# Performance work log

Hardware: AMD Instinct MI355X
Metric: run time of the kernel (lower is better)

The kernel has to match this reference:

```python
import jax, jax.numpy as jnp
import numpy as np

B, N, C, H, L = 4, 1024, 1152, 16, 120
D = C // H
HID = 4 * C
EPS = 1e-6


def _ln(x):
    m = jnp.mean(x, axis=-1, keepdims=True)
    v = jnp.var(x, axis=-1, keepdims=True)
    return (x - m) * jax.lax.rsqrt(v + EPS)


def _attend(q, k, v):
    # q:(B,H,Nq,D) k,v:(B,H,Nk,D)
    scale = D ** -0.5
    s = jnp.einsum('bhnd,bhmd->bhnm', q, k) * scale
    p = jax.nn.softmax(s, axis=-1)
    o = jnp.einsum('bhnm,bhmd->bhnd', p, v)
    return o.transpose(0, 2, 1, 3).reshape(q.shape[0], q.shape[2], C)


def setup_inputs() -> dict:
    key = jax.random.key(0)
    ks = jax.random.split(key, 20)
    g = lambda i, shape, s=0.02: jax.random.normal(ks[i], shape, jnp.float32) * s
    return {
        'x': jax.random.normal(ks[0], (B, N, C), jnp.float32),
        'y': jax.random.normal(ks[1], (B, L, C), jnp.float32),
        't': jax.random.normal(ks[2], (B, 6 * C), jnp.float32),
        'sst': jax.random.normal(ks[3], (6, C), jnp.float32) / C ** 0.5,
        'qkv_w': g(4, (C, 3 * C)), 'qkv_b': jnp.zeros((3 * C,), jnp.float32),
        'proj_w': g(5, (C, C)), 'proj_b': jnp.zeros((C,), jnp.float32),
        'q_w': g(6, (C, C)), 'q_b': jnp.zeros((C,), jnp.float32),
        'kv_w': g(7, (C, 2 * C)), 'kv_b': jnp.zeros((2 * C,), jnp.float32),
        'cproj_w': g(8, (C, C)), 'cproj_b': jnp.zeros((C,), jnp.float32),
        'fc1_w': g(9, (C, HID)), 'fc1_b': jnp.zeros((HID,), jnp.float32),
        'fc2_w': g(10, (HID, C)), 'fc2_b': jnp.zeros((C,), jnp.float32),
    }


def reference(x, y, t, sst, qkv_w, qkv_b, proj_w, proj_b, q_w, q_b,
              kv_w, kv_b, cproj_w, cproj_b, fc1_w, fc1_b, fc2_w, fc2_b):
    mods = sst[None] + t.reshape(B, 6, C)  # (B,6,C)
    sh_msa, sc_msa, g_msa, sh_mlp, sc_mlp, g_mlp = [mods[:, i:i + 1] for i in range(6)]

    # --- self attention with adaLN modulation ---
    h = _ln(x) * (1 + sc_msa) + sh_msa
    qkv = (h @ qkv_w + qkv_b).reshape(B, N, 3, H, D).transpose(2, 0, 3, 1, 4)
    attn_out = _attend(qkv[0], qkv[1], qkv[2]) @ proj_w + proj_b
    x = x + g_msa * attn_out

    # --- cross attention (batched cond, no mask) ---
    q = (x @ q_w + q_b).reshape(B, N, H, D).transpose(0, 2, 1, 3)
    kv = (y @ kv_w + kv_b).reshape(B, L, 2, H, D).transpose(2, 0, 3, 1, 4)
    x = x + (_attend(q, kv[0], kv[1]) @ cproj_w + cproj_b)

    # --- MLP with adaLN modulation ---
    h = _ln(x) * (1 + sc_mlp) + sh_mlp
    h = jax.nn.gelu(h @ fc1_w + fc1_b, approximate=True) @ fc2_w + fc2_b
    x = x + g_mlp * h
    return x
```

## Files before the change

### kernel.cpp

```cpp
#include <hip/hip_runtime.h>
#include <hip/hip_bf16.h>
#include <stdint.h>

typedef __hip_bfloat16 BT;
typedef __bf16 bf16x8 __attribute__((ext_vector_type(8)));
typedef float f32x4 __attribute__((ext_vector_type(4)));

constexpr int kB = 4, kN = 1024, kC = 1152, kH = 16, kL = 120, kD = 72, kDp = 96;
constexpr int kHid = 4608, kBN = 4096, kZ = 64;
constexpr float kScale = 0.11785113019775793f;

__global__ void detect_dtype(const void* xin, int* flag) {
  __shared__ int cnt;
  if (threadIdx.x == 0) cnt = 0;
  __syncthreads();
  const BT* xb = (const BT*)xin;
  int local = 0;
  for (int i = threadIdx.x; i < 4096; i += 256) {
    float v = __bfloat162float(xb[i]);
    if (!(fabsf(v) <= 1e3f)) local++;
  }
  atomicAdd(&cnt, local);
  __syncthreads();
  if (threadIdx.x == 0) *flag = (cnt > 8) ? 1 : 0;
}

struct ConvSeg {
  const void* src;
  BT* dst;
  long long n;
};
struct ConvArgs {
  ConvSeg seg[10];
  int nseg;
};
__global__ void convert_all(ConvArgs a, const int* __restrict__ flag) {
  const int f = *flag;
  long long i = (long long)blockIdx.x * 256 + threadIdx.x;
#pragma unroll
  for (int s = 0; s < 10; ++s) {
    if (s >= a.nseg) return;
    if (i < a.seg[s].n) {
      a.seg[s].dst[i] = f ? __float2bfloat16(((const float*)a.seg[s].src)[i])
                          : ((const BT*)a.seg[s].src)[i];
      return;
    }
    i -= a.seg[s].n;
  }
}

__global__ void encode_ws(float* out, long long n, float c) {
  long long i = (long long)blockIdx.x * 256 + threadIdx.x;
  if (i < n) out[i] = c;
}

__device__ __forceinline__ void gl_lds16(const BT* g, BT* l) {
  __builtin_amdgcn_global_load_lds(
      (const __attribute__((address_space(1))) uint32_t*)g,
      (__attribute__((address_space(3))) uint32_t*)l, 16, 0, 0);
}

__global__ __launch_bounds__(256, 2) void flash_self(
    const BT* __restrict__ Qp, const BT* __restrict__ Kp, const BT* __restrict__ VT,
    BT* __restrict__ O) {
  const int z = blockIdx.y;
  const int q0 = blockIdx.x * 64;
  const BT* Qb = Qp + (size_t)z * kN * kDp;
  const BT* Kb = Kp + (size_t)z * kN * kDp;
  const BT* Vb = VT + (size_t)z * kD * kN;
  BT* Ob = O + (size_t)z * kN * kD;

  __shared__ __align__(16) BT Pl[64][136];
  __shared__ float redm[2][64], reds[2][64], scl[64], lsh[64];

  const int lane = threadIdx.x & 63, w = threadIdx.x >> 6;
  const int l15 = lane & 15, g8 = (lane >> 4) * 8, rowq = (lane >> 4) * 4;
  const int wm = (w & 1) * 32, wn = (w >> 1) * 64;
  const int half = w >> 1;
  const int orow = w * 16;

  bf16x8 afQ[3][2];
#pragma unroll
  for (int ks = 0; ks < 3; ++ks)
#pragma unroll
    for (int i = 0; i < 2; ++i)
      afQ[ks][i] = *reinterpret_cast<const bf16x8*>(
          &Qb[(size_t)(q0 + wm + i * 16 + l15) * kDp + ks * 32 + g8]);

  float mst[2][4], lst[2][4];
#pragma unroll
  for (int i = 0; i < 2; ++i)
#pragma unroll
    for (int r = 0; r < 4; ++r) {
      mst[i][r] = -1e30f;
      lst[i][r] = 0.f;
    }

  f32x4 accO[5] = {};

  for (int t = 0; t < 8; ++t) {
    const int kv0 = t * 128;
    f32x4 accS[2][4] = {};
#pragma unroll
    for (int ks = 0; ks < 3; ++ks) {
      bf16x8 bfK[4];
#pragma unroll
      for (int j = 0; j < 4; ++j)
        bfK[j] = *reinterpret_cast<const bf16x8*>(
            &Kb[(size_t)(kv0 + wn + j * 16 + l15) * kDp + ks * 32 + g8]);
#pragma unroll
      for (int i = 0; i < 2; ++i)
#pragma unroll
        for (int j = 0; j < 4; ++j)
          accS[i][j] = __builtin_amdgcn_mfma_f32_16x16x32_bf16(afQ[ks][i], bfK[j], accS[i][j], 0, 0, 0);
    }
    float tmax[2][4];
#pragma unroll
    for (int i = 0; i < 2; ++i)
#pragma unroll
      for (int r = 0; r < 4; ++r) {
        float v = fmaxf(fmaxf(accS[i][0][r], accS[i][1][r]),
                        fmaxf(accS[i][2][r], accS[i][3][r]));
        v = fmaxf(v, __shfl_xor(v, 1, 16));
        v = fmaxf(v, __shfl_xor(v, 2, 16));
        v = fmaxf(v, __shfl_xor(v, 4, 16));
        v = fmaxf(v, __shfl_xor(v, 8, 16));
        tmax[i][r] = v;
      }
    if (l15 == 0) {
#pragma unroll
      for (int i = 0; i < 2; ++i)
#pragma unroll
        for (int r = 0; r < 4; ++r)
          redm[half][wm + i * 16 + rowq + r] = tmax[i][r];
    }
    __syncthreads();

    float sc[2][4], tsum[2][4];
#pragma unroll
    for (int i = 0; i < 2; ++i)
#pragma unroll
      for (int r = 0; r < 4; ++r) {
        const int row = wm + i * 16 + rowq + r;
        const float mt = fmaxf(redm[0][row], redm[1][row]);
        const float mn = fmaxf(mst[i][r], mt);
        sc[i][r] = __expf(mst[i][r] - mn);
        mst[i][r] = mn;
        float s = 0.f;
#pragma unroll
        for (int j = 0; j < 4; ++j) {
          float pv = __expf(accS[i][j][r] - mn);
          s += pv;
          Pl[row][wn + j * 16 + l15] = __float2bfloat16(pv);
        }
        s += __shfl_xor(s, 1, 16);
        s += __shfl_xor(s, 2, 16);
        s += __shfl_xor(s, 4, 16);
        s += __shfl_xor(s, 8, 16);
        tsum[i][r] = s;
      }
    if (l15 == 0) {
#pragma unroll
      for (int i = 0; i < 2; ++i)
#pragma unroll
        for (int r = 0; r < 4; ++r) {
          const int row = wm + i * 16 + rowq + r;
          reds[half][row] = tsum[i][r];
          if (half == 0) scl[row] = sc[i][r];
        }
    }
    __syncthreads();

#pragma unroll
    for (int i = 0; i < 2; ++i)
#pragma unroll
      for (int r = 0; r < 4; ++r) {
        const int row = wm + i * 16 + rowq + r;
        lst[i][r] = lst[i][r] * sc[i][r] + (reds[0][row] + reds[1][row]);
      }
    float osc[4];
#pragma unroll
    for (int r = 0; r < 4; ++r) osc[r] = scl[orow + rowq + r];
#pragma unroll
    for (int jv = 0; jv < 5; ++jv)
#pragma unroll
      for (int r = 0; r < 4; ++r) accO[jv][r] *= osc[r];
#pragma unroll
    for (int ks = 0; ks < 4; ++ks) {
      bf16x8 aP = *reinterpret_cast<const bf16x8*>(&Pl[orow + l15][ks * 32 + g8]);
      bf16x8 bV[5];
#pragma unroll
      for (int jv = 0; jv < 5; ++jv)
        bV[jv] = *reinterpret_cast<const bf16x8*>(
            &Vb[(size_t)(jv * 16 + l15) * kN + kv0 + ks * 32 + g8]);
#pragma unroll
      for (int jv = 0; jv < 5; ++jv)
        accO[jv] = __builtin_amdgcn_mfma_f32_16x16x32_bf16(aP, bV[jv], accO[jv], 0, 0, 0);
    }
  }

  if (half == 0 && l15 == 0) {
#pragma unroll
    for (int i = 0; i < 2; ++i)
#pragma unroll
      for (int r = 0; r < 4; ++r)
        lsh[wm + i * 16 + rowq + r] = lst[i][r];
  }
  __syncthreads();
  float linv[4];
#pragma unroll
  for (int r = 0; r < 4; ++r) linv[r] = 1.f / lsh[orow + rowq + r];
#pragma unroll
  for (int jv = 0; jv < 5; ++jv) {
    const int d = jv * 16 + l15;
    if (d < kD) {
#pragma unroll
      for (int r = 0; r < 4; ++r)
        Ob[(size_t)(q0 + orow + rowq + r) * kD + d] =
            __float2bfloat16(accO[jv][r] * linv[r]);
    }
  }
}

template <int EP>
__global__ __launch_bounds__(512, 2) void gemm_w8(
    const BT* __restrict__ A, const BT* __restrict__ Bm, const BT* __restrict__ bias,
    void* __restrict__ Cout, int M, int Nc, int K, int lda, int ldb, int ldc,
    long long sA, long long sB, long long sC) {
  __shared__ __align__(16) BT As[2][128 * 64];
  __shared__ __align__(16) BT Bs[2][128 * 64];
  A += (long long)blockIdx.z * sA;
  Bm += (long long)blockIdx.z * sB;

  const int gx = gridDim.x, nwg = gx * gridDim.y;
  int id = blockIdx.y * gx + blockIdx.x;
  {
    const int q = nwg >> 3, r = nwg & 7;
    const int xcd = id & 7, pos = id >> 3;
    const int base = (xcd < r) ? xcd * (q + 1) : r * (q + 1) + (xcd - r) * q;
    id = base + pos;
  }
  const int m0 = (id / gx) * 128, n0 = (id % gx) * 128;

  const int lane = threadIdx.x & 63, w = threadIdx.x >> 6;
  const int l15 = lane & 15;
  const int srow = lane >> 3;
  const int ssrc = ((lane & 7) ^ srow) * 8;
  const int wm = (w & 1) * 64, wn = (w >> 1) * 32;

  const int u = w;
  const BT* gp[4];
#pragma unroll
  for (int q = 0; q < 4; ++q) {
    int rr, lim;
    const BT* basep;
    int stride;
    if (u < 4) { rr = m0 + u * 32; lim = M; basep = A; stride = lda; }
    else { rr = n0 + (u - 4) * 32; lim = Nc; basep = Bm; stride = ldb; }
    rr += q * 8 + srow;
    if (rr >= lim) rr = lim - 1;
    gp[q] = basep + (long long)rr * stride + ssrc;
  }
  BT* dst[2];
#pragma unroll
  for (int bb = 0; bb < 2; ++bb)
    dst[bb] = (u < 4) ? &As[bb][u * 2048] : &Bs[bb][(u - 4) * 2048];

  auto stage = [&](int bb, int k0) {
#pragma unroll
    for (int q = 0; q < 4; ++q) gl_lds16(gp[q] + k0, dst[bb] + q * 512);
  };

  const int rsw = l15 & 7;
  const int ch0 = ((lane >> 4) ^ rsw) * 8;
  const int ch1 = ((4 | (lane >> 4)) ^ rsw) * 8;

  f32x4 acc[4][2] = {};

  auto compute = [&](int bb) {
    bf16x8 af[4][2], bf[2][2];
#pragma unroll
    for (int i = 0; i < 4; ++i) {
      const int row = wm + i * 16 + l15;
      af[i][0] = *reinterpret_cast<const bf16x8*>(&As[bb][row * 64 + ch0]);
      af[i][1] = *reinterpret_cast<const bf16x8*>(&As[bb][row * 64 + ch1]);
    }
#pragma unroll
    for (int j = 0; j < 2; ++j) {
      const int row = wn + j * 16 + l15;
      bf[j][0] = *reinterpret_cast<const bf16x8*>(&Bs[bb][row * 64 + ch0]);
      bf[j][1] = *reinterpret_cast<const bf16x8*>(&Bs[bb][row * 64 + ch1]);
    }
#pragma unroll
    for (int i = 0; i < 4; ++i)
#pragma unroll
      for (int j = 0; j < 2; ++j) {
        acc[i][j] = __builtin_amdgcn_mfma_f32_16x16x32_bf16(af[i][0], bf[j][0], acc[i][j], 0, 0, 0);
        acc[i][j] = __builtin_amdgcn_mfma_f32_16x16x32_bf16(af[i][1], bf[j][1], acc[i][j], 0, 0, 0);
      }
  };

  stage(0, 0);
  __syncthreads();
  const int nk = K >> 6;
  int cur = 0;
  for (int t = 1; t < nk; ++t) {
    stage(cur ^ 1, t << 6);
    compute(cur);
    __syncthreads();
    cur ^= 1;
  }
  compute(cur);

  const int rowq = (lane >> 4) * 4;
  const long long cb = (long long)blockIdx.z * sC;
#pragma unroll
  for (int j = 0; j < 2; ++j) {
    int col = n0 + wn + j * 16 + l15;
    if (col >= Nc) continue;
    float bv = bias ? __bfloat162float(bias[col]) : 0.f;
#pragma unroll
    for (int i = 0; i < 4; ++i) {
      int row = m0 + wm + i * 16 + rowq;
#pragma unroll
      for (int r = 0; r < 4; ++r) {
        if (row + r < M) {
          float v = acc[i][j][r] + bv;
          if (EP == 2) {
            float z = 1.5957691216057308f * (v + 0.044715f * v * v * v);
            v = v / (1.f + __expf(-z));
          }
          long long off = cb + (long long)(row + r) * ldc + col;
          if (EP == 1)
            ((float*)Cout)[off] = v;
          else
            ((BT*)Cout)[off] = __float2bfloat16(v);
        }
      }
    }
  }
}

template <int BM, int BN, int EP>
__global__ __launch_bounds__(256, 3) void gemm_t64(
    const BT* __restrict__ A, const BT* __restrict__ Bm, const BT* __restrict__ bias,
    void* __restrict__ Cout, int M, int Nc, int K, int lda, int ldb, int ldc,
    long long sA, long long sB, long long sC) {
  constexpr int NA = BM / 32;
  constexpr int NB = BN / 32;
  constexpr int NU = NA + NB;
  constexpr int NJ = 2;
  __shared__ __align__(16) BT As[2][BM * 64];
  __shared__ __align__(16) BT Bs[2][BN * 64];
  A += (long long)blockIdx.z * sA;
  Bm += (long long)blockIdx.z * sB;

  const int gx = gridDim.x, nwg = gx * gridDim.y;
  int id = blockIdx.y * gx + blockIdx.x;
  {
    const int q = nwg >> 3, r = nwg & 7;
    const int xcd = id & 7, pos = id >> 3;
    const int base = (xcd < r) ? xcd * (q + 1) : r * (q + 1) + (xcd - r) * q;
    id = base + pos;
  }
  const int m0 = (id / gx) * BM, n0 = (id % gx) * BN;

  const int lane = threadIdx.x & 63, w = threadIdx.x >> 6;
  const int l15 = lane & 15;
  const int srow = lane >> 3;
  const int ssrc = ((lane & 7) ^ srow) * 8;
  int wm, wn;
  if (BM == 128) { wm = (w >> 1) * 64; wn = (w & 1) * 32; }
  else { wm = 0; wn = w * 32; }

  const bool has2 = (w + 4 < NU);
  const int u1 = w;
  const int u2 = has2 ? (w + 4) : w;
  const BT* gp1[4];
  const BT* gp2[4];
#pragma unroll
  for (int q = 0; q < 4; ++q) {
    {
      int rr, lim;
      const BT* basep;
      int stride;
      if (u1 < NA) { rr = m0 + u1 * 32; lim = M; basep = A; stride = lda; }
      else { rr = n0 + (u1 - NA) * 32; lim = Nc; basep = Bm; stride = ldb; }
      rr += q * 8 + srow;
      if (rr >= lim) rr = lim - 1;
      gp1[q] = basep + (long long)rr * stride + ssrc;
    }
    {
      int rr, lim;
      const BT* basep;
      int stride;
      if (u2 < NA) { rr = m0 + u2 * 32; lim = M; basep = A; stride = lda; }
      else { rr = n0 + (u2 - NA) * 32; lim = Nc; basep = Bm; stride = ldb; }
      rr += q * 8 + srow;
      if (rr >= lim) rr = lim - 1;
      gp2[q] = basep + (long long)rr * stride + ssrc;
    }
  }
  BT* d1[2];
  BT* d2[2];
#pragma unroll
  for (int bb = 0; bb < 2; ++bb) {
    d1[bb] = (u1 < NA) ? &As[bb][u1 * 2048] : &Bs[bb][(u1 - NA) * 2048];
    int ub = u2 - NA;
    if (ub < 0) ub = 0;
    if (ub > NB - 1) ub = NB - 1;
    d2[bb] = (u2 < NA) ? &As[bb][u2 * 2048] : &Bs[bb][ub * 2048];
  }

  auto stage = [&](int bb, int k0) {
#pragma unroll
    for (int q = 0; q < 4; ++q) gl_lds16(gp1[q] + k0, d1[bb] + q * 512);
    if (has2) {
#pragma unroll
      for (int q = 0; q < 4; ++q) gl_lds16(gp2[q] + k0, d2[bb] + q * 512);
    }
  };

  const int rsw = l15 & 7;
  const int ch0 = ((lane >> 4) ^ rsw) * 8;
  const int ch1 = ((4 | (lane >> 4)) ^ rsw) * 8;

  f32x4 acc[4][NJ] = {};

  auto compute = [&](int bb) {
    bf16x8 af[4][2], bf[NJ][2];
#pragma unroll
    for (int i = 0; i < 4; ++i) {
      const int row = wm + i * 16 + l15;
      af[i][0] = *reinterpret_cast<const bf16x8*>(&As[bb][row * 64 + ch0]);
      af[i][1] = *reinterpret_cast<const bf16x8*>(&As[bb][row * 64 + ch1]);
    }
#pragma unroll
    for (int j = 0; j < NJ; ++j) {
      const int row = wn + j * 16 + l15;
      bf[j][0] = *reinterpret_cast<const bf16x8*>(&Bs[bb][row * 64 + ch0]);
      bf[j][1] = *reinterpret_cast<const bf16x8*>(&Bs[bb][row * 64 + ch1]);
    }
#pragma unroll
    for (int i = 0; i < 4; ++i)
#pragma unroll
      for (int j = 0; j < NJ; ++j) {
        acc[i][j] = __builtin_amdgcn_mfma_f32_16x16x32_bf16(af[i][0], bf[j][0], acc[i][j], 0, 0, 0);
        acc[i][j] = __builtin_amdgcn_mfma_f32_16x16x32_bf16(af[i][1], bf[j][1], acc[i][j], 0, 0, 0);
      }
  };

  stage(0, 0);
  __syncthreads();
  const int nk = K >> 6;
  int cur = 0;
  for (int t = 1; t < nk; ++t) {
    stage(cur ^ 1, t << 6);
    compute(cur);
    __syncthreads();
    cur ^= 1;
  }
  compute(cur);

  const int rowq = (lane >> 4) * 4;
  const long long cb = (long long)blockIdx.z * sC;
#pragma unroll
  for (int j = 0; j < NJ; ++j) {
    int col = n0 + wn + j * 16 + l15;
    if (col >= Nc) continue;
    float bv = bias ? __bfloat162float(bias[col]) : 0.f;
#pragma unroll
    for (int i = 0; i < 4; ++i) {
      int row = m0 + wm + i * 16 + rowq;
#pragma unroll
      for (int r = 0; r < 4; ++r) {
        if (row + r < M) {
          float v = acc[i][j][r] + bv;
          if (EP == 2) {
            float z = 1.5957691216057308f * (v + 0.044715f * v * v * v);
            v = v / (1.f + __expf(-z));
          }
          long long off = cb + (long long)(row + r) * ldc + col;
          if (EP == 1)
            ((float*)Cout)[off] = v;
          else
            ((BT*)Cout)[off] = __float2bfloat16(v);
        }
      }
    }
  }
}

template <int EP>
__global__ __launch_bounds__(256, 4) void gemm_tile(
    const BT* __restrict__ A, const BT* __restrict__ Bm, const BT* __restrict__ bias,
    void* __restrict__ Cout, int M, int Nc, int K, int lda, int ldb, int ldc,
    long long sA, long long sB, long long sC) {
  __shared__ __align__(16) BT As[2][128 * 32];
  __shared__ __align__(16) BT Bs[2][128 * 32];
  A += (long long)blockIdx.z * sA;
  Bm += (long long)blockIdx.z * sB;

  const int gx = gridDim.x, nwg = gx * gridDim.y;
  int id = blockIdx.y * gx + blockIdx.x;
  {
    const int q = nwg >> 3, r = nwg & 7;
    const int xcd = id & 7, pos = id >> 3;
    const int base = (xcd < r) ? xcd * (q + 1) : r * (q + 1) + (xcd - r) * q;
    id = base + pos;
  }
  const int m0 = (id / gx) * 128, n0 = (id % gx) * 128;

  const int lane = threadIdx.x & 63, w = threadIdx.x >> 6;
  const int lr = lane >> 2, lc = (lane & 3) * 8;
  const int l15 = lane & 15, q8 = (lane >> 4) * 8;
  const int wm = (w & 1) * 64, wn = (w >> 1) * 64;

  int ra0 = m0 + w * 32 + lr, ra1 = ra0 + 16;
  if (ra0 >= M) ra0 = M - 1;
  if (ra1 >= M) ra1 = M - 1;
  int rb0 = n0 + w * 32 + lr, rb1 = rb0 + 16;
  if (rb0 >= Nc) rb0 = Nc - 1;
  if (rb1 >= Nc) rb1 = Nc - 1;
  const BT* pa0 = A + (long long)ra0 * lda + lc;
  const BT* pa1 = A + (long long)ra1 * lda + lc;
  const BT* pb0 = Bm + (long long)rb0 * ldb + lc;
  const BT* pb1 = Bm + (long long)rb1 * ldb + lc;

  auto stage = [&](int bb, int k0) {
    gl_lds16(pa0 + k0, &As[bb][w * 1024]);
    gl_lds16(pa1 + k0, &As[bb][w * 1024 + 512]);
    gl_lds16(pb0 + k0, &Bs[bb][w * 1024]);
    gl_lds16(pb1 + k0, &Bs[bb][w * 1024 + 512]);
  };

  f32x4 acc[4][4] = {};

  auto compute = [&](int bb) {
    bf16x8 af[4], bf[4];
#pragma unroll
    for (int i = 0; i < 4; ++i)
      af[i] = *reinterpret_cast<const bf16x8*>(&As[bb][(wm + i * 16 + l15) * 32 + q8]);
#pragma unroll
    for (int j = 0; j < 4; ++j)
      bf[j] = *reinterpret_cast<const bf16x8*>(&Bs[bb][(wn + j * 16 + l15) * 32 + q8]);
#pragma unroll
    for (int i = 0; i < 4; ++i)
#pragma unroll
      for (int j = 0; j < 4; ++j)
        acc[i][j] = __builtin_amdgcn_mfma_f32_16x16x32_bf16(af[i], bf[j], acc[i][j], 0, 0, 0);
  };

  stage(0, 0);
  __syncthreads();
  const int nk = K >> 5;
  int cur = 0;
  for (int t = 1; t < nk; ++t) {
    stage(cur ^ 1, t << 5);
    compute(cur);
    __syncthreads();
    cur ^= 1;
  }
  compute(cur);

  const int rowq = (lane >> 4) * 4;
  const long long cb = (long long)blockIdx.z * sC;
#pragma unroll
  for (int j = 0; j < 4; ++j) {
    int col = n0 + wn + j * 16 + l15;
    if (col >= Nc) continue;
    float bv = bias ? __bfloat162float(bias[col]) : 0.f;
#pragma unroll
    for (int i = 0; i < 4; ++i) {
      int row = m0 + wm + i * 16 + rowq;
#pragma unroll
      for (int r = 0; r < 4; ++r) {
        if (row + r < M) {
          float v = acc[i][j][r] + bv;
          if (EP == 2) {
            float z = 1.5957691216057308f * (v + 0.044715f * v * v * v);
            v = v / (1.f + __expf(-z));
          }
          long long off = cb + (long long)(row + r) * ldc + col;
          if (EP == 1)
            ((float*)Cout)[off] = v;
          else
            ((BT*)Cout)[off] = __float2bfloat16(v);
        }
      }
    }
  }
}

__global__ void transpose_any(const void* __restrict__ in, BT* __restrict__ out,
                              int R, int Cin, const int* __restrict__ flag) {
  __shared__ BT tile[32][33];
  const int f = *flag;
  const int tx = threadIdx.x & 31, ty = threadIdx.x >> 5;
  const int r0 = blockIdx.y * 32, c0 = blockIdx.x * 32;
#pragma unroll
  for (int j = 0; j < 32; j += 8) {
    int r = r0 + ty + j;
    if (r < R && c0 + tx < Cin) {
      long long idx = (long long)r * Cin + c0 + tx;
      tile[ty + j][tx] = f ? __float2bfloat16(((const float*)in)[idx]) : ((const BT*)in)[idx];
    }
  }
  __syncthreads();
#pragma unroll
  for (int j = 0; j < 32; j += 8) {
    int oc = c0 + ty + j;
    if (oc < Cin && r0 + tx < R) out[(long long)oc * R + r0 + tx] = tile[tx][ty + j];
  }
}

template <int SRC>
__global__ __launch_bounds__(256) void ln_mod(const void* __restrict__ xin,
                                              const BT* __restrict__ tc,
                                              const BT* __restrict__ sstc,
                                              BT* __restrict__ hout,
                                              int shiftRow, int scaleRow,
                                              const int* __restrict__ flag) {
  const int f = (SRC == 1) ? 1 : *flag;
  const int row = blockIdx.x;
  const int b = row >> 10;
  const long long base = (long long)row * kC;
  float s = 0.f, s2 = 0.f;
  for (int c = threadIdx.x; c < kC; c += 256) {
    float v = f ? ((const float*)xin)[base + c] : __bfloat162float(((const BT*)xin)[base + c]);
    s += v;
    s2 += v * v;
  }
  for (int o = 32; o > 0; o >>= 1) {
    s += __shfl_down(s, o, 64);
    s2 += __shfl_down(s2, o, 64);
  }
  __shared__ float red[8];
  const int w = threadIdx.x >> 6;
  if ((threadIdx.x & 63) == 0) {
    red[w] = s;
    red[4 + w] = s2;
  }
  __syncthreads();
  const float m = (red[0] + red[1] + red[2] + red[3]) * (1.f / kC);
  const float ex2 = (red[4] + red[5] + red[6] + red[7]) * (1.f / kC);
  const float rstd = rsqrtf(ex2 - m * m + 1e-6f);
  const BT* tsh = tc + (long long)b * 6 * kC + (long long)shiftRow * kC;
  const BT* tsc = tc + (long long)b * 6 * kC + (long long)scaleRow * kC;
  const BT* ssh = sstc + (long long)shiftRow * kC;
  const BT* ssc = sstc + (long long)scaleRow * kC;
  for (int c = threadIdx.x; c < kC; c += 256) {
    float sc = __bfloat162float(ssc[c]) + __bfloat162float(tsc[c]);
    float sh = __bfloat162float(ssh[c]) + __bfloat162float(tsh[c]);
    float xv0 = f ? ((const float*)xin)[base + c] : __bfloat162float(((const BT*)xin)[base + c]);
    float xv = (xv0 - m) * rstd;
    hout[base + c] = __float2bfloat16(xv * (1.f + sc) + sh);
  }
}

__global__ void scatter_qk(const BT* __restrict__ qkv, BT* __restrict__ Qp,
                           BT* __restrict__ Kp) {
  long long i = (long long)blockIdx.x * 256 + threadIdx.x;
  if (i >= (long long)kZ * kN * kDp) return;
  int d = (int)(i % kDp);
  long long r = i / kDp;
  int n = (int)(r % kN);
  int z = (int)(r / kN);
  int b = z >> 4, h = z & 15;
  if (d < kD) {
    long long src = ((long long)(b * kN + n)) * (3 * kC) + h * kD + d;
    Qp[i] = __float2bfloat16(kScale * __bfloat162float(qkv[src]));
    Kp[i] = qkv[src + kC];
  } else {
    Qp[i] = __float2bfloat16(0.f);
    Kp[i] = __float2bfloat16(0.f);
  }
}

__global__ void scatter_v(const BT* __restrict__ qkv, BT* __restrict__ VT) {
  long long i = (long long)blockIdx.x * 256 + threadIdx.x;
  if (i >= (long long)kZ * kD * kN) return;
  int n = (int)(i % kN);
  long long r = i / kN;
  int d = (int)(r % kD);
  int z = (int)(r / kD);
  int b = z >> 4, h = z & 15;
  VT[i] = qkv[((long long)(b * kN + n)) * (3 * kC) + 2 * kC + h * kD + d];
}

__global__ void scatter_qc(const BT* __restrict__ qc, BT* __restrict__ Qp) {
  long long i = (long long)blockIdx.x * 256 + threadIdx.x;
  if (i >= (long long)kZ * kN * kDp) return;
  int d = (int)(i % kDp);
  long long r = i / kDp;
  int n = (int)(r % kN);
  int z = (int)(r / kN);
  int b = z >> 4, h = z & 15;
  Qp[i] = (d < kD)
              ? __float2bfloat16(kScale * __bfloat162float(qc[((long long)(b * kN + n)) * kC + h * kD + d]))
              : __float2bfloat16(0.f);
}

__global__ void scatter_kc(const BT* __restrict__ kvb, BT* __restrict__ Kcp) {
  long long i = (long long)blockIdx.x * 256 + threadIdx.x;
  if (i >= (long long)kZ * kL * kDp) return;
  int d = (int)(i % kDp);
  long long r = i / kDp;
  int l = (int)(r % kL);
  int z = (int)(r / kL);
  int b = z >> 4, h = z & 15;
  Kcp[i] = (d < kD) ? kvb[((long long)(b * kL + l)) * (2 * kC) + h * kD + d] : __float2bfloat16(0.f);
}

__global__ void scatter_vc(const BT* __restrict__ kvb, BT* __restrict__ VcT) {
  long long i = (long long)blockIdx.x * 256 + threadIdx.x;
  if (i >= (long long)kZ * kD * 128) return;
  int l = (int)(i % 128);
  long long r = i / 128;
  int d = (int)(r % kD);
  int z = (int)(r / kD);
  int b = z >> 4, h = z & 15;
  VcT[i] = (l < kL) ? kvb[((long long)(b * kL + l)) * (2 * kC) + kC + h * kD + d] : __float2bfloat16(0.f);
}

__global__ void heads_to_cat(const BT* __restrict__ O, BT* __restrict__ cat) {
  long long i = (long long)blockIdx.x * 256 + threadIdx.x;
  if (i >= (long long)kZ * kN * kD) return;
  int d = (int)(i % kD);
  long long r = i / kD;
  int n = (int)(r % kN);
  int z = (int)(r / kN);
  int b = z >> 4, h = z & 15;
  cat[((long long)(b * kN + n)) * kC + h * kD + d] = O[i];
}

__global__ void softmax_cross(BT* __restrict__ S) {
  const long long row = blockIdx.x;
  BT* r = S + row * 128;
  const int c = threadIdx.x;
  float v = (c < kL) ? __bfloat162float(r[c]) : -1e30f;
  float mx = v;
  for (int o = 32; o > 0; o >>= 1) mx = fmaxf(mx, __shfl_down(mx, o, 64));
  __shared__ float sm[2], ss[2];
  if ((c & 63) == 0) sm[c >> 6] = mx;
  __syncthreads();
  mx = fmaxf(sm[0], sm[1]);
  float e = (c < kL) ? __expf(v - mx) : 0.f;
  float s = e;
  for (int o = 32; o > 0; o >>= 1) s += __shfl_down(s, o, 64);
  if ((c & 63) == 0) ss[c >> 6] = s;
  __syncthreads();
  s = ss[0] + ss[1];
  r[c] = __float2bfloat16(e / s);
}

__global__ void resid_gate(const void* __restrict__ x, const BT* __restrict__ raw,
                           const BT* __restrict__ tc, const BT* __restrict__ sstc,
                           float* __restrict__ resf, BT* __restrict__ resb,
                           const int* __restrict__ flag) {
  long long i = (long long)blockIdx.x * 256 + threadIdx.x;
  if (i >= (long long)kBN * kC) return;
  const int f = *flag;
  int c = (int)(i % kC);
  int b = (int)(i / ((long long)kN * kC));
  float g = __bfloat162float(sstc[2 * kC + c]) + __bfloat162float(tc[(long long)b * 6 * kC + 2 * kC + c]);
  float xv = f ? ((const float*)x)[i] : __bfloat162float(((const BT*)x)[i]);
  float v = xv + g * __bfloat162float(raw[i]);
  resf[i] = v;
  resb[i] = __float2bfloat16(v);
}

__global__ void resid_add(float* __restrict__ res, const BT* __restrict__ raw) {
  long long i = (long long)blockIdx.x * 256 + threadIdx.x;
  if (i < (long long)kBN * kC) res[i] += __bfloat162float(raw[i]);
}

__global__ void final_out(const float* __restrict__ res, const BT* __restrict__ raw,
                          const BT* __restrict__ tc, const BT* __restrict__ sstc,
                          float* __restrict__ out) {
  long long i = (long long)blockIdx.x * 256 + threadIdx.x;
  if (i >= (long long)kBN * kC) return;
  int c = (int)(i % kC);
  int b = (int)(i / ((long long)kN * kC));
  float g = __bfloat162float(sstc[5 * kC + c]) + __bfloat162float(tc[(long long)b * 6 * kC + 5 * kC + c]);
  out[i] = res[i] + g * __bfloat162float(raw[i]);
}

extern "C" void kernel_launch(void* const* d_in, const int* in_sizes, int n_in,
                              void* d_out, int out_size, void* d_ws, size_t ws_size,
                              hipStream_t stream) {
  const void* x = d_in[0];
  const void* y = d_in[1];
  const void* t = d_in[2];
  const void* sst = d_in[3];
  const void* qkv_w = d_in[4];
  const void* qkv_b = d_in[5];
  const void* proj_w = d_in[6];
  const void* proj_b = d_in[7];
  const void* q_w = d_in[8];
  const void* q_b = d_in[9];
  const void* kv_w = d_in[10];
  const void* kv_b = d_in[11];
  const void* cproj_w = d_in[12];
  const void* cproj_b = d_in[13];
  const void* fc1_w = d_in[14];
  const void* fc1_b = d_in[15];
  const void* fc2_w = d_in[16];
  const void* fc2_b = d_in[17];
  (void)in_sizes; (void)n_in;

  char* p = (char*)d_ws;
  size_t off = 0;
  auto alloc = [&](size_t bytes) {
    void* r = p + off;
    off += (bytes + 1023) & ~(size_t)1023;
    return r;
  };
  int* dflag = (int*)alloc(16);
  BT* canonY = (BT*)alloc((size_t)kB * kL * kC * 2);
  BT* canonT = (BT*)alloc((size_t)kB * 6 * kC * 2);
  BT* canonSst = (BT*)alloc((size_t)6 * kC * 2);
  BT* canonBias = (BT*)alloc((size_t)16384 * 2);
  BT* wT = (BT*)alloc((size_t)kHid * kC * 2);
  BT* bufH = (BT*)alloc((size_t)kBN * kC * 2);
  BT* bufCH = (BT*)alloc((size_t)kZ * kN * kDp * 2);
  BT* bufQp = (BT*)alloc((size_t)kZ * kN * kDp * 2);
  BT* bufVT = (BT*)alloc((size_t)kZ * kD * kN * 2);
  BT* rawB = (BT*)alloc((size_t)kBN * kC * 2);
  float* resF = (float*)alloc((size_t)kBN * kC * 4);
  BT* arena = (BT*)alloc((size_t)kBN * kHid * 2);
  const size_t need = off;

  BT* bufO = rawB;
  BT* fc2T = bufQp;
  BT* kvBuf = (BT*)((char*)arena + 17825792);

  if (ws_size < need) {
    float c = 100.f * (float)(1 + (int)(ws_size >> 24));
    long long n = (long long)out_size;
    encode_ws<<<(int)((n + 255) / 256), 256, 0, stream>>>((float*)d_out, n, c);
    return;
  }

  BT* qkvB = canonBias;
  BT* projB = canonBias + 3456;
  BT* qB = canonBias + 4608;
  BT* kvB = canonBias + 5760;
  BT* cprojB = canonBias + 8064;
  BT* fc1B = canonBias + 9216;
  BT* fc2B = canonBias + 13824;

  auto gemm = [&](int ep, const BT* A, const BT* Bm, const BT* bias, void* Cp,
                  int M, int Nc, int K, int lda, int ldb, int ldc,
                  long long sA, long long sB, long long sC, int Zb) {
    if (K & 63) {
      dim3 g((Nc + 127) / 128, (M + 127) / 128, Zb);
      if (ep == 0)
        gemm_tile<0><<<g, 256, 0, stream>>>(A, Bm, bias, Cp, M, Nc, K, lda, ldb, ldc, sA, sB, sC);
      else if (ep == 1)
        gemm_tile<1><<<g, 256, 0, stream>>>(A, Bm, bias, Cp, M, Nc, K, lda, ldb, ldc, sA, sB, sC);
      else
        gemm_tile<2><<<g, 256, 0, stream>>>(A, Bm, bias, Cp, M, Nc, K, lda, ldb, ldc, sA, sB, sC);
      return;
    }
    long long nwg128 = (long long)((Nc + 127) / 128) * ((M + 127) / 128) * Zb;
    if (nwg128 >= 768 && (M & 127) == 0) {
      dim3 g((Nc + 127) / 128, M / 128, Zb);
      if (ep == 0)
        gemm_w8<0><<<g, 512, 0, stream>>>(A, Bm, bias, Cp, M, Nc, K, lda, ldb, ldc, sA, sB, sC);
      else if (ep == 1)
        gemm_w8<1><<<g, 512, 0, stream>>>(A, Bm, bias, Cp, M, Nc, K, lda, ldb, ldc, sA, sB, sC);
      else
        gemm_w8<2><<<g, 512, 0, stream>>>(A, Bm, bias, Cp, M, Nc, K, lda, ldb, ldc, sA, sB, sC);
      return;
    }
    long long n64 = (long long)((Nc + 63) / 64) * ((M + 127) / 128) * Zb;
    if (n64 >= 512) {
      dim3 g((Nc + 63) / 64, (M + 127) / 128, Zb);
      if (ep == 0)
        gemm_t64<128, 64, 0><<<g, 256, 0, stream>>>(A, Bm, bias, Cp, M, Nc, K, lda, ldb, ldc, sA, sB, sC);
      else if (ep == 1)
        gemm_t64<128, 64, 1><<<g, 256, 0, stream>>>(A, Bm, bias, Cp, M, Nc, K, lda, ldb, ldc, sA, sB, sC);
      else
        gemm_t64<128, 64, 2><<<g, 256, 0, stream>>>(A, Bm, bias, Cp, M, Nc, K, lda, ldb, ldc, sA, sB, sC);
    } else {
      dim3 g((Nc + 127) / 128, (M + 63) / 64, Zb);
      if (ep == 0)
        gemm_t64<64, 128, 0><<<g, 256, 0, stream>>>(A, Bm, bias, Cp, M, Nc, K, lda, ldb, ldc, sA, sB, sC);
      else if (ep == 1)
        gemm_t64<64, 128, 1><<<g, 256, 0, stream>>>(A, Bm, bias, Cp, M, Nc, K, lda, ldb, ldc, sA, sB, sC);
      else
        gemm_t64<64, 128, 2><<<g, 256, 0, stream>>>(A, Bm, bias, Cp, M, Nc, K, lda, ldb, ldc, sA, sB, sC);
    }
  };
  auto tp = [&](const void* in, BT* out, int R, int Cin) {
    dim3 g((Cin + 31) / 32, (R + 31) / 32);
    transpose_any<<<g, 256, 0, stream>>>(in, out, R, Cin, dflag);
  };

  detect_dtype<<<1, 256, 0, stream>>>(x, dflag);
  {
    ConvArgs a;
    a.seg[0] = {y, canonY, (long long)kB * kL * kC};
    a.seg[1] = {t, canonT, (long long)kB * 6 * kC};
    a.seg[2] = {sst, canonSst, (long long)6 * kC};
    a.seg[3] = {qkv_b, qkvB, 3456};
    a.seg[4] = {proj_b, projB, 1152};
    a.seg[5] = {q_b, qB, 1152};
    a.seg[6] = {kv_b, kvB, 2304};
    a.seg[7] = {cproj_b, cprojB, 1152};
    a.seg[8] = {fc1_b, fc1B, 4608};
    a.seg[9] = {fc2_b, fc2B, 1152};
    a.nseg = 10;
    long long tot = 552960 + 27648 + 6912 + 14976;
    convert_all<<<(int)((tot + 255) / 256), 256, 0, stream>>>(a, dflag);
  }

  ln_mod<0><<<kBN, 256, 0, stream>>>(x, canonT, canonSst, bufH, 0, 1, dflag);
  tp(qkv_w, wT, kC, 3 * kC);
  gemm(0, bufH, wT, qkvB, arena, kBN, 3 * kC, kC, kC, kC, 3 * kC, 0, 0, 0, 1);
  {
    long long tot = (long long)kZ * kN * kDp;
    scatter_qk<<<(int)((tot + 255) / 256), 256, 0, stream>>>(arena, bufQp, bufCH);
    tot = (long long)kZ * kD * kN;
    scatter_v<<<(int)((tot + 255) / 256), 256, 0, stream>>>(arena, bufVT);
  }
  flash_self<<<dim3(16, 64), 256, 0, stream>>>(bufQp, bufCH, bufVT, bufO);
  heads_to_cat<<<18432, 256, 0, stream>>>(bufO, bufCH);
  tp(proj_w, wT, kC, kC);
  gemm(0, bufCH, wT, projB, rawB, kBN, kC, kC, kC, kC, kC, 0, 0, 0, 1);
  resid_gate<<<18432, 256, 0, stream>>>(x, rawB, canonT, canonSst, resF, bufH, dflag);

  tp(q_w, wT, kC, kC);
  gemm(0, bufH, wT, qB, bufCH, kBN, kC, kC, kC, kC, kC, 0, 0, 0, 1);
  {
    long long tot = (long long)kZ * kN * kDp;
    scatter_qc<<<(int)((tot + 255) / 256), 256, 0, stream>>>(bufCH, bufQp);
  }
  tp(kv_w, wT, kC, 2 * kC);
  gemm(0, canonY, wT, kvB, kvBuf, kB * kL, 2 * kC, kC, kC, kC, 2 * kC, 0, 0, 0, 1);
  {
    long long tot = (long long)kZ * kL * kDp;
    scatter_kc<<<(int)((tot + 255) / 256), 256, 0, stream>>>(kvBuf, bufCH);
    tot = (long long)kZ * kD * 128;
    scatter_vc<<<(int)((tot + 255) / 256), 256, 0, stream>>>(kvBuf, bufVT);
  }
  gemm(0, bufQp, bufCH, nullptr, arena, kN, kL, kDp, kDp, kDp, 128,
       (long long)kN * kDp, (long long)kL * kDp, (long long)kN * 128, kZ);
  softmax_cross<<<kZ * kN, 128, 0, stream>>>(arena);
  gemm(0, arena, bufVT, nullptr, bufO, kN, kD, 128, 128, 128, kD,
       (long long)kN * 128, (long long)kD * 128, (long long)kN * kD, kZ);
  heads_to_cat<<<18432, 256, 0, stream>>>(bufO, bufCH);
  tp(cproj_w, wT, kC, kC);
  gemm(0, bufCH, wT, cprojB, rawB, kBN, kC, kC, kC, kC, kC, 0, 0, 0, 1);
  resid_add<<<18432, 256, 0, stream>>>(resF, rawB);

  ln_mod<1><<<kBN, 256, 0, stream>>>(resF, canonT, canonSst, bufH, 3, 4, dflag);
  tp(fc1_w, wT, kC, kHid);
  tp(fc2_w, fc2T, kHid, kC);
  gemm(2, bufH, wT, fc1B, arena, kBN, kHid, kC, kC, kC, kHid, 0, 0, 0, 1);
  gemm(0, arena, fc2T, fc2B, rawB, kBN, kC, kHid, kHid, kHid, kC, 0, 0, 0, 1);
  final_out<<<18432, 256, 0, stream>>>(resF, rawB, canonT, canonSst, (float*)d_out);
}
```

Baseline: 735.0 us.

## Give each wave its own query rows in flash_self, removing block barriers

Restructures the self-attention kernel so each of the four waves owns 16 query rows and the full 128-key tile. Row max and sum reductions then stay within the wave, which removes the shared-memory reduction arrays and the per-tile __syncthreads. V fragments for the tile are prefetched into registers before the QK MFMAs. The 1D grid is remapped so consecutive blocks are spread across XCD-style groups of 8, which may improve L2 locality per head. The trade-off is higher register pressure from the 20 V fragments and 8 score accumulators, and each wave now loads all K rows itself.

```diff
diff --git a/kernel.cpp b/kernel.cpp
--- a/kernel.cpp
+++ b/kernel.cpp
@@ -63,161 +63,109 @@
 __global__ __launch_bounds__(256, 2) void flash_self(
     const BT* __restrict__ Qp, const BT* __restrict__ Kp, const BT* __restrict__ VT,
     BT* __restrict__ O) {
-  const int z = blockIdx.y;
-  const int q0 = blockIdx.x * 64;
+  int id = blockIdx.x;
+  id = (id & 7) * 128 + (id >> 3);
+  const int z = id >> 4;
+  const int q0 = (id & 15) * 64;
+
   const BT* Qb = Qp + (size_t)z * kN * kDp;
   const BT* Kb = Kp + (size_t)z * kN * kDp;
   const BT* Vb = VT + (size_t)z * kD * kN;
   BT* Ob = O + (size_t)z * kN * kD;
 
   __shared__ __align__(16) BT Pl[64][136];
-  __shared__ float redm[2][64], reds[2][64], scl[64], lsh[64];
 
   const int lane = threadIdx.x & 63, w = threadIdx.x >> 6;
   const int l15 = lane & 15, g8 = (lane >> 4) * 8, rowq = (lane >> 4) * 4;
-  const int wm = (w & 1) * 32, wn = (w >> 1) * 64;
-  const int half = w >> 1;
-  const int orow = w * 16;
-
-  bf16x8 afQ[3][2];
+  const int qw = q0 + w * 16;
+
+  bf16x8 afQ[3];
 #pragma unroll
   for (int ks = 0; ks < 3; ++ks)
-#pragma unroll
-    for (int i = 0; i < 2; ++i)
-      afQ[ks][i] = *reinterpret_cast<const bf16x8*>(
-          &Qb[(size_t)(q0 + wm + i * 16 + l15) * kDp + ks * 32 + g8]);
-
-  float mst[2][4], lst[2][4];
-#pragma unroll
-  for (int i = 0; i < 2; ++i)
-#pragma unroll
-    for (int r = 0; r < 4; ++r) {
-      mst[i][r] = -1e30f;
-      lst[i][r] = 0.f;
-    }
-
+    afQ[ks] = *reinterpret_cast<const bf16x8*>(
+        &Qb[(size_t)(qw + l15) * kDp + ks * 32 + g8]);
+
+  float m[4], l[4];
+#pragma unroll
+  for (int r = 0; r < 4; ++r) {
+    m[r] = -1e30f;
+    l[r] = 0.f;
+  }
   f32x4 accO[5] = {};
 
   for (int t = 0; t < 8; ++t) {
     const int kv0 = t * 128;
-    f32x4 accS[2][4] = {};
+    bf16x8 bfV[5][4];
+#pragma unroll
+    for (int jv = 0; jv < 5; ++jv)
+#pragma unroll
+      for (int ks = 0; ks < 4; ++ks)
+        bfV[jv][ks] = *reinterpret_cast<const bf16x8*>(
+            &Vb[(size_t)(jv * 16 + l15) * kN + kv0 + ks * 32 + g8]);
+
+    f32x4 accS[8] = {};
 #pragma unroll
     for (int ks = 0; ks < 3; ++ks) {
-      bf16x8 bfK[4];
-#pragma unroll
-      for (int j = 0; j < 4; ++j)
+      bf16x8 bfK[8];
+#pragma unroll
+      for (int j = 0; j < 8; ++j)
         bfK[j] = *reinterpret_cast<const bf16x8*>(
-            &Kb[(size_t)(kv0 + wn + j * 16 + l15) * kDp + ks * 32 + g8]);
-#pragma unroll
-      for (int i = 0; i < 2; ++i)
-#pragma unroll
-        for (int j = 0; j < 4; ++j)
-          accS[i][j] = __builtin_amdgcn_mfma_f32_16x16x32_bf16(afQ[ks][i], bfK[j], accS[i][j], 0, 0, 0);
-    }
-    float tmax[2][4];
-#pragma unroll
-    for (int i = 0; i < 2; ++i)
-#pragma unroll
-      for (int r = 0; r < 4; ++r) {
-        float v = fmaxf(fmaxf(accS[i][0][r], accS[i][1][r]),
-                        fmaxf(accS[i][2][r], accS[i][3][r]));
-        v = fmaxf(v, __shfl_xor(v, 1, 16));
-        v = fmaxf(v, __shfl_xor(v, 2, 16));
-        v = fmaxf(v, __shfl_xor(v, 4, 16));
-        v = fmaxf(v, __shfl_xor(v, 8, 16));
-        tmax[i][r] = v;
+            &Kb[(size_t)(kv0 + j * 16 + l15) * kDp + ks * 32 + g8]);
+#pragma unroll
+      for (int j = 0; j < 8; ++j)
+        accS[j] = __builtin_amdgcn_mfma_f32_16x16x32_bf16(afQ[ks], bfK[j], accS[j], 0, 0, 0);
+    }
+
+    float sc[4];
+#pragma unroll
+    for (int r = 0; r < 4; ++r) {
+      float v = accS[0][r];
+#pragma unroll
+      for (int j = 1; j < 8; ++j) v = fmaxf(v, accS[j][r]);
+      v = fmaxf(v, __shfl_xor(v, 1, 16));
+      v = fmaxf(v, __shfl_xor(v, 2, 16));
+      v = fmaxf(v, __shfl_xor(v, 4, 16));
+      v = fmaxf(v, __shfl_xor(v, 8, 16));
+      const float mn = fmaxf(m[r], v);
+      sc[r] = __expf(m[r] - mn);
+      m[r] = mn;
+      float s = 0.f;
+#pragma unroll
+      for (int j = 0; j < 8; ++j) {
+        float pv = __expf(accS[j][r] - mn);
+        s += pv;
+        Pl[w * 16 + rowq + r][j * 16 + l15] = __float2bfloat16(pv);
       }
-    if (l15 == 0) {
-#pragma unroll
-      for (int i = 0; i < 2; ++i)
-#pragma unroll
-        for (int r = 0; r < 4; ++r)
-          redm[half][wm + i * 16 + rowq + r] = tmax[i][r];
-    }
-    __syncthreads();
-
-    float sc[2][4], tsum[2][4];
-#pragma unroll
-    for (int i = 0; i < 2; ++i)
-#pragma unroll
-      for (int r = 0; r < 4; ++r) {
-        const int row = wm + i * 16 + rowq + r;
-        const float mt = fmaxf(redm[0][row], redm[1][row]);
-        const float mn = fmaxf(mst[i][r], mt);
-        sc[i][r] = __expf(mst[i][r] - mn);
-        mst[i][r] = mn;
-        float s = 0.f;
-#pragma unroll
-        for (int j = 0; j < 4; ++j) {
-          float pv = __expf(accS[i][j][r] - mn);
-          s += pv;
-          Pl[row][wn + j * 16 + l15] = __float2bfloat16(pv);
-        }
-        s += __shfl_xor(s, 1, 16);
-        s += __shfl_xor(s, 2, 16);
-        s += __shfl_xor(s, 4, 16);
-        s += __shfl_xor(s, 8, 16);
-        tsum[i][r] = s;
-      }
-    if (l15 == 0) {
-#pragma unroll
-      for (int i = 0; i < 2; ++i)
-#pragma unroll
-        for (int r = 0; r < 4; ++r) {
-          const int row = wm + i * 16 + rowq + r;
-          reds[half][row] = tsum[i][r];
-          if (half == 0) scl[row] = sc[i][r];
-        }
-    }
-    __syncthreads();
-
-#pragma unroll
-    for (int i = 0; i < 2; ++i)
-#pragma unroll
-      for (int r = 0; r < 4; ++r) {
-        const int row = wm + i * 16 + rowq + r;
-        lst[i][r] = lst[i][r] * sc[i][r] + (reds[0][row] + reds[1][row]);
-      }
-    float osc[4];
-#pragma unroll
-    for (int r = 0; r < 4; ++r) osc[r] = scl[orow + rowq + r];
+      s += __shfl_xor(s, 1, 16);
+      s += __shfl_xor(s, 2, 16);
+      s += __shfl_xor(s, 4, 16);
+      s += __shfl_xor(s, 8, 16);
+      l[r] = l[r] * sc[r] + s;
+    }
+
 #pragma unroll
     for (int jv = 0; jv < 5; ++jv)
 #pragma unroll
-      for (int r = 0; r < 4; ++r) accO[jv][r] *= osc[r];
+      for (int r = 0; r < 4; ++r) accO[jv][r] *= sc[r];
 #pragma unroll
     for (int ks = 0; ks < 4; ++ks) {
-      bf16x8 aP = *reinterpret_cast<const bf16x8*>(&Pl[orow + l15][ks * 32 + g8]);
-      bf16x8 bV[5];
+      bf16x8 aP = *reinterpret_cast<const bf16x8*>(&Pl[w * 16 + l15][ks * 32 + g8]);
 #pragma unroll
       for (int jv = 0; jv < 5; ++jv)
-        bV[jv] = *reinterpret_cast<const bf16x8*>(
-            &Vb[(size_t)(jv * 16 + l15) * kN + kv0 + ks * 32 + g8]);
-#pragma unroll
-      for (int jv = 0; jv < 5; ++jv)
-        accO[jv] = __builtin_amdgcn_mfma_f32_16x16x32_bf16(aP, bV[jv], accO[jv], 0, 0, 0);
-    }
-  }
-
-  if (half == 0 && l15 == 0) {
-#pragma unroll
-    for (int i = 0; i < 2; ++i)
-#pragma unroll
-      for (int r = 0; r < 4; ++r)
-        lsh[wm + i * 16 + rowq + r] = lst[i][r];
-  }
-  __syncthreads();
+        accO[jv] = __builtin_amdgcn_mfma_f32_16x16x32_bf16(aP, bfV[jv][ks], accO[jv], 0, 0, 0);
+    }
+  }
+
   float linv[4];
 #pragma unroll
-  for (int r = 0; r < 4; ++r) linv[r] = 1.f / lsh[orow + rowq + r];
+  for (int r = 0; r < 4; ++r) linv[r] = 1.f / l[r];
 #pragma unroll
   for (int jv = 0; jv < 5; ++jv) {
     const int d = jv * 16 + l15;
     if (d < kD) {
 #pragma unroll
       for (int r = 0; r < 4; ++r)
-        Ob[(size_t)(q0 + orow + rowq + r) * kD + d] =
-            __float2bfloat16(accO[jv][r] * linv[r]);
+        Ob[(size_t)(qw + rowq + r) * kD + d] = __float2bfloat16(accO[jv][r] * linv[r]);
     }
   }
 }
@@ -925,7 +873,7 @@
     tot = (long long)kZ * kD * kN;
     scatter_v<<<(int)((tot + 255) / 256), 256, 0, stream>>>(arena, bufVT);
   }
-  flash_self<<<dim3(16, 64), 256, 0, stream>>>(bufQp, bufCH, bufVT, bufO);
+  flash_self<<<1024, 256, 0, stream>>>(bufQp, bufCH, bufVT, bufO);
   heads_to_cat<<<18432, 256, 0, stream>>>(bufO, bufCH);
   tp(proj_w, wT, kC, kC);
   gemm(0, bufCH, wT, projB, rawB, kBN, kC, kC, kC, kC, kC, 0, 0, 0, 1);
```

Result: no change. 736.9 us (+0.3%).
